# Optimization experiments

Measured on AMD Instinct MI355X. Metric: run time of the kernel, lower is better.

The kernel has to match this reference:

```python
import jax, jax.numpy as jnp
import numpy as np

GAMMA = 0.99
GAE_LAMBDA = 0.95
CLIP = 0.2
ENT_COEF = 0.01
VF_COEF = 0.5


def setup_inputs() -> dict:
    key = jax.random.key(0)
    ks = jax.random.split(key, 12)
    T, D, H, A = 65536, 512, 256, 16
    obs = jax.random.normal(ks[0], (T, D), dtype=jnp.float32)
    actions = jax.random.randint(ks[1], (T,), 0, A, dtype=jnp.int32)
    logprobs = jax.random.normal(ks[2], (T,), dtype=jnp.float32)
    rewards = jax.random.normal(ks[3], (T,), dtype=jnp.float32)
    terms = jax.random.uniform(ks[4], (T,), dtype=jnp.float32)
    values = jax.random.normal(ks[5], (T,), dtype=jnp.float32)
    # orthogonal-init-like scaling (std sqrt(2) for trunk, 0.01 actor, 1.0 critic)
    W1 = jax.random.normal(ks[6], (D, H), dtype=jnp.float32) * np.float32(np.sqrt(2.0 / D))
    b1 = jnp.zeros((H,), jnp.float32)
    W2 = jax.random.normal(ks[7], (H, H), dtype=jnp.float32) * np.float32(np.sqrt(2.0 / H))
    b2 = jnp.zeros((H,), jnp.float32)
    Wa = jax.random.normal(ks[8], (H, A), dtype=jnp.float32) * np.float32(0.01 / np.sqrt(H))
    ba = jnp.zeros((A,), jnp.float32)
    Wc = jax.random.normal(ks[9], (H, 1), dtype=jnp.float32) * np.float32(1.0 / np.sqrt(H))
    bc = jnp.zeros((1,), jnp.float32)
    return {"obs": obs, "actions": actions, "logprobs": logprobs, "rewards": rewards,
            "terms": terms, "values": values, "W1": W1, "b1": b1, "W2": W2, "b2": b2,
            "Wa": Wa, "ba": ba, "Wc": Wc, "bc": bc}


def reference(obs, actions, logprobs, rewards, terms, values,
              W1, b1, W2, b2, Wa, ba, Wc, bc):
    # ---- GAE (torch.no_grad in original -> stop_gradient) ----
    nonterm = 1.0 - terms                                   # [T]
    next_vals = jnp.concatenate([values[1:], jnp.zeros((1,), values.dtype)])
    delta = rewards + GAMMA * next_vals * nonterm - values  # [T]

    def step(carry, x):  # reverse recurrence a_t = d_t + g*l*nt_t * a_{t+1}
        d, nt = x
        g = d + GAMMA * GAE_LAMBDA * nt * carry
        return g, g

    _, adv = jax.lax.scan(step, jnp.float32(0.0), (delta, nonterm), reverse=True)
    adv = jax.lax.stop_gradient(adv)
    returns = adv + jax.lax.stop_gradient(values)
    vals_old = jax.lax.stop_gradient(values)

    # ---- actor-critic MLP (get_action_and_value) ----
    hidden = jnp.tanh(jnp.tanh(obs @ W1 + b1) @ W2 + b2)    # [T,256]
    logits = hidden @ Wa + ba                               # [T,A]
    logp = jax.nn.log_softmax(logits, axis=-1)
    newlp = jnp.take_along_axis(logp, actions[:, None].astype(jnp.int32), axis=1)[:, 0]
    entropy = -jnp.sum(jnp.exp(logp) * logp, axis=-1)       # [T]
    value = (hidden @ Wc + bc)[:, 0]                        # [T]

    # ---- clipped PPO losses (single full-batch minibatch) ----
    ratio = jnp.exp(newlp - logprobs)
    a = (adv - adv.mean()) / (adv.std() + 1e-8)
    pg_loss = jnp.maximum(-a * ratio, -a * jnp.clip(ratio, 1.0 - CLIP, 1.0 + CLIP)).mean()
    v_clipped = vals_old + jnp.clip(value - vals_old, -CLIP, CLIP)
    v_loss = 0.5 * jnp.maximum((value - returns) ** 2, (v_clipped - returns) ** 2).mean()
    loss = pg_loss - ENT_COEF * entropy.mean() + VF_COEF * v_loss
    return loss
```

## Files before the change

### kernel.cpp

```cpp
#include <hip/hip_runtime.h>


#define TT 65536

typedef float f32x4 __attribute__((ext_vector_type(4)));
typedef __bf16 bf16x8 __attribute__((ext_vector_type(8)));
typedef unsigned short u16x8 __attribute__((ext_vector_type(8)));

__device__ __forceinline__ unsigned short f2bf(float f) {
    unsigned int u = __float_as_uint(f);
    unsigned int r = (u + 0x7fffu + ((u >> 16) & 1u)) >> 16;
    return (unsigned short)r;
}

__device__ __forceinline__ float fast_tanh(float x) {
    float e = __expf(2.0f * x);
    return fmaf(-2.0f, __builtin_amdgcn_rcpf(e + 1.0f), 1.0f);
}

__device__ __forceinline__ void suffix_scan256(float* sC, float* sD, int i) {
    float c = sC[i], d = sD[i];
#pragma unroll
    for (int s = 1; s < 256; s <<= 1) {
        float c2 = 1.0f, d2 = 0.0f;
        if (i + s < 256) { c2 = sC[i + s]; d2 = sD[i + s]; }
        __syncthreads();
        d = d + c * d2;
        c = c * c2;
        sC[i] = c; sD[i] = d;
        __syncthreads();
    }
}

__device__ __forceinline__ void gae_cd(const float* rewards, const float* terms,
                                       const float* values, int t, float* c, float* d) {
    float nt = 1.0f - terms[t];
    float nv = (t + 1 < TT) ? values[t + 1] : 0.0f;
    *d = rewards[t] + 0.99f * nv * nt - values[t];
    *c = 0.99f * 0.95f * nt;
}

__global__ void k_prep_gae1(const float* __restrict__ W1, const float* __restrict__ W2,
                            const float* __restrict__ Wa, const float* __restrict__ Wc,
                            unsigned short* __restrict__ W1T, unsigned short* __restrict__ W2T,
                            unsigned short* __restrict__ WavT,
                            const float* __restrict__ rewards, const float* __restrict__ terms,
                            const float* __restrict__ values, float* __restrict__ aggC,
                            float* __restrict__ aggD) {
    if (blockIdx.x < 800) {
        int idx = blockIdx.x * 256 + threadIdx.x;
        if (idx < 131072) {
            int n = idx >> 9, k = idx & 511;
            W1T[idx] = f2bf(W1[k * 256 + n]);
        } else if (idx < 196608) {
            int i = idx - 131072;
            int n = i >> 8, k = i & 255;
            W2T[i] = f2bf(W2[k * 256 + n]);
        } else if (idx < 204800) {
            int i = idx - 196608;
            int r = i >> 8, k = i & 255;
            float v = (r < 16) ? Wa[k * 16 + r] : ((r == 16) ? Wc[k] : 0.0f);
            WavT[i] = f2bf(v);
        }
        return;
    }
    __shared__ float sC[256], sD[256];
    int i = threadIdx.x;
    int b = blockIdx.x - 800;
    int t = b * 256 + i;
    float c, d;
    gae_cd(rewards, terms, values, t, &c, &d);
    sC[i] = c; sD[i] = d;
    __syncthreads();
    suffix_scan256(sC, sD, i);
    if (i == 0) { aggC[b] = sC[0]; aggD[b] = sD[0]; }
}

__global__ void k_gae3(const float* __restrict__ rewards, const float* __restrict__ terms,
                       const float* __restrict__ values, const float* __restrict__ aggC,
                       const float* __restrict__ aggD, float* __restrict__ adv,
                       float* __restrict__ ret, float* __restrict__ sumP) {
    __shared__ float sC[256], sD[256];
    int i = threadIdx.x, b = blockIdx.x;
    sC[i] = aggC[i]; sD[i] = aggD[i];
    __syncthreads();
    suffix_scan256(sC, sD, i);
    float carry = (b < 255) ? sD[b + 1] : 0.0f;
    __syncthreads();

    int t = b * 256 + i;
    float c, d;
    gae_cd(rewards, terms, values, t, &c, &d);
    sC[i] = c; sD[i] = d;
    __syncthreads();
    suffix_scan256(sC, sD, i);
    float a = sD[i] + sC[i] * carry;
    adv[t] = a;
    ret[t] = a + values[t];
    __syncthreads();
    sC[i] = a; sD[i] = a * a;
    __syncthreads();
#pragma unroll
    for (int s = 128; s > 0; s >>= 1) {
        if (i < s) { sC[i] += sC[i + s]; sD[i] += sD[i + s]; }
        __syncthreads();
    }
    if (i == 0) { sumP[2 * b] = sC[0]; sumP[2 * b + 1] = sD[0]; }
}

__global__ __launch_bounds__(1024, 4) void k_mlp(
    const float* __restrict__ obs, const int* __restrict__ actions,
    const float* __restrict__ logprobs, const float* __restrict__ values,
    const float* __restrict__ b1, const float* __restrict__ b2,
    const float* __restrict__ ba, const float* __restrict__ bc,
    const unsigned short* __restrict__ W1T, const unsigned short* __restrict__ W2T,
    const unsigned short* __restrict__ WavT, const float* __restrict__ adv,
    const float* __restrict__ ret, const float* __restrict__ sumP,
    float* __restrict__ lossP) {
    __shared__ __align__(16) unsigned char SM[147456];
    unsigned short* smH = (unsigned short*)SM;
    unsigned short* smB2 = (unsigned short*)(SM + 131072);
    float* red = (float*)SM;

    const int tid = threadIdx.x;
    const int wid = tid >> 6;
    const int lane = tid & 63;
    const int cl = lane & 15;
    const int gg = lane >> 4;
    const int mw = wid >> 2;
    const int nw = wid & 3;
    const int bm0 = blockIdx.x * 256;

    const int srow = tid >> 2;
    const int sslot = tid & 3;
    const int sdst = srow * 32 + (((sslot ^ ((srow >> 1) & 3))) << 3);

    unsigned short* smB1b[2] = {(unsigned short*)SM, (unsigned short*)(SM + 16384)};
    unsigned short* smAb[2]  = {(unsigned short*)(SM + 32768), (unsigned short*)(SM + 49152)};

    const float* aSrc = obs + (size_t)(bm0 + srow) * 512 + sslot * 8;
    float4 ar0, ar1;
    u16x8 brf;
    ar0 = *(const float4*)(aSrc);
    ar1 = *(const float4*)(aSrc + 4);
    brf = *(const u16x8*)(W1T + srow * 512 + sslot * 8);

    float meanA, rstdA;
    {
        if (tid < 256) { red[tid] = sumP[2 * tid]; red[256 + tid] = sumP[2 * tid + 1]; }
        __syncthreads();
#pragma unroll
        for (int s = 128; s > 0; s >>= 1) {
            if (tid < s) { red[tid] += red[tid + s]; red[256 + tid] += red[256 + tid + s]; }
            __syncthreads();
        }
        meanA = red[0] * (1.0f / TT);
        float var = red[256] * (1.0f / TT) - meanA * meanA;
        rstdA = 1.0f / (sqrtf(fmaxf(var, 0.0f)) + 1e-8f);
        __syncthreads();
    }

    float b1v[4], b2v[4];
#pragma unroll
    for (int n = 0; n < 4; ++n) {
        int c = nw * 64 + n * 16 + cl;
        b1v[n] = b1[c];
        b2v[n] = b2[c];
    }
    const float bav = ba[cl];
    const float bc0 = bc[0];

    f32x4 acc[4][4];
#pragma unroll
    for (int m = 0; m < 4; ++m)
#pragma unroll
        for (int n = 0; n < 4; ++n) acc[m][n] = (f32x4){0.f, 0.f, 0.f, 0.f};

    auto cvtWriteA = [&](const float4& f0, const float4& f1, unsigned short* dst) {
        u16x8 cc;
        cc[0] = f2bf(f0.x); cc[1] = f2bf(f0.y); cc[2] = f2bf(f0.z); cc[3] = f2bf(f0.w);
        cc[4] = f2bf(f1.x); cc[5] = f2bf(f1.y); cc[6] = f2bf(f1.z); cc[7] = f2bf(f1.w);
        *(u16x8*)(dst + sdst) = cc;
    };

    cvtWriteA(ar0, ar1, smAb[0]);
    *(u16x8*)(smB1b[0] + sdst) = brf;
    __syncthreads();

    u16x8 b2rf;
#pragma unroll
    for (int t = 0; t < 16; ++t) {
        if (t < 15) {
            ar0 = *(const float4*)(aSrc + (t + 1) * 32);
            ar1 = *(const float4*)(aSrc + (t + 1) * 32 + 4);
            brf = *(const u16x8*)(W1T + srow * 512 + (t + 1) * 32 + sslot * 8);
        } else {
            b2rf = *(const u16x8*)(W2T + srow * 256 + sslot * 8);
        }
        bf16x8 av[4], bv[4];
#pragma unroll
        for (int m = 0; m < 4; ++m) {
            int ra = mw * 64 + m * 16 + cl;
            av[m] = *(const bf16x8*)&smAb[t & 1][ra * 32 + ((gg ^ ((ra >> 1) & 3)) << 3)];
        }
#pragma unroll
        for (int n = 0; n < 4; ++n) {
            int rb = nw * 64 + n * 16 + cl;
            bv[n] = *(const bf16x8*)&smB1b[t & 1][rb * 32 + ((gg ^ ((rb >> 1) & 3)) << 3)];
        }
#pragma unroll
        for (int m = 0; m < 4; ++m)
#pragma unroll
            for (int n = 0; n < 4; ++n)
                acc[m][n] = __builtin_amdgcn_mfma_f32_16x16x32_bf16(av[m], bv[n], acc[m][n], 0, 0, 0);
        if (t < 15) {
            cvtWriteA(ar0, ar1, smAb[(t + 1) & 1]);
            *(u16x8*)(smB1b[(t + 1) & 1] + sdst) = brf;
        }
        __syncthreads();
    }

#pragma unroll
    for (int m = 0; m < 4; ++m)
#pragma unroll
        for (int n = 0; n < 4; ++n)
#pragma unroll
            for (int j = 0; j < 4; ++j) {
                int r = mw * 64 + m * 16 + gg * 4 + j;
                int c = nw * 64 + n * 16 + cl;
                smH[r * 256 + (c ^ ((r & 7) << 3))] = f2bf(fast_tanh(acc[m][n][j] + b1v[n]));
                acc[m][n][j] = 0.0f;
            }
    *(u16x8*)(smB2 + sdst) = b2rf;
    __syncthreads();

    u16x8 wvrf;
#pragma unroll
    for (int t = 0; t < 8; ++t) {
        if (t < 7) b2rf = *(const u16x8*)(W2T + srow * 256 + (t + 1) * 32 + sslot * 8);
        else       wvrf = *(const u16x8*)(WavT + (tid >> 5) * 256 + (tid & 31) * 8);
        bf16x8 av[4], bv[4];
#pragma unroll
        for (int m = 0; m < 4; ++m) {
            int ra = mw * 64 + m * 16 + cl;
            av[m] = *(const bf16x8*)&smH[ra * 256 + ((t * 32 + gg * 8) ^ ((ra & 7) << 3))];
        }
#pragma unroll
        for (int n = 0; n < 4; ++n) {
            int rb = nw * 64 + n * 16 + cl;
            bv[n] = *(const bf16x8*)&smB2[rb * 32 + ((gg ^ ((rb >> 1) & 3)) << 3)];
        }
#pragma unroll
        for (int m = 0; m < 4; ++m)
#pragma unroll
            for (int n = 0; n < 4; ++n)
                acc[m][n] = __builtin_amdgcn_mfma_f32_16x16x32_bf16(av[m], bv[n], acc[m][n], 0, 0, 0);
        __syncthreads();
        if (t < 7) {
            *(u16x8*)(smB2 + sdst) = b2rf;
            __syncthreads();
        }
    }

#pragma unroll
    for (int m = 0; m < 4; ++m)
#pragma unroll
        for (int n = 0; n < 4; ++n)
#pragma unroll
            for (int j = 0; j < 4; ++j) {
                int r = mw * 64 + m * 16 + gg * 4 + j;
                int c = nw * 64 + n * 16 + cl;
                smH[r * 256 + (c ^ ((r & 7) << 3))] = f2bf(fast_tanh(acc[m][n][j] + b2v[n]));
            }
    {
        int wrow = tid >> 5, we = (tid & 31) * 8;
        *(u16x8*)(smB2 + wrow * 256 + (we ^ ((wrow & 7) << 3))) = wvrf;
    }
    __syncthreads();

    f32x4 acc_a = {0.f, 0.f, 0.f, 0.f}, acc_v = {0.f, 0.f, 0.f, 0.f};
#pragma unroll
    for (int kk = 0; kk < 8; ++kk) {
        int r = wid * 16 + cl;
        bf16x8 av = *(const bf16x8*)&smH[r * 256 + ((kk * 32 + gg * 8) ^ ((r & 7) << 3))];
        int ra2 = cl;
        bf16x8 bva = *(const bf16x8*)&smB2[ra2 * 256 + ((kk * 32 + gg * 8) ^ ((ra2 & 7) << 3))];
        int rv = 16 + cl;
        bf16x8 bvv = *(const bf16x8*)&smB2[rv * 256 + ((kk * 32 + gg * 8) ^ ((rv & 7) << 3))];
        acc_a = __builtin_amdgcn_mfma_f32_16x16x32_bf16(av, bva, acc_a, 0, 0, 0);
        acc_v = __builtin_amdgcn_mfma_f32_16x16x32_bf16(av, bvv, acc_v, 0, 0, 0);
    }

    float lsum = 0.0f;
    const int t0 = bm0 + wid * 16;
#pragma unroll
    for (int j = 0; j < 4; ++j) {
        int t = t0 + gg * 4 + j;
        float lg = acc_a[j] + bav;
        float mx = lg;
#pragma unroll
        for (int dd = 1; dd < 16; dd <<= 1) mx = fmaxf(mx, __shfl_xor(mx, dd));
        float ex = __expf(lg - mx);
        float se = ex;
#pragma unroll
        for (int dd = 1; dd < 16; dd <<= 1) se += __shfl_xor(se, dd);
        float ls = __logf(se);
        float lp = lg - mx - ls;
        float pl = __expf(lp) * lp;
        float ent = pl;
#pragma unroll
        for (int dd = 1; dd < 16; dd <<= 1) ent += __shfl_xor(ent, dd);
        ent = -ent;
        int act = actions[t];
        float newlp = __shfl(lp, (lane & 48) | act);
        float val = __shfl(acc_v[j], lane & 48) + bc0;

        float lpo = logprobs[t];
        float at = (adv[t] - meanA) * rstdA;
        float rt = ret[t];
        float vo = values[t];
        float ratio = __expf(newlp - lpo);
        float rcl = fminf(fmaxf(ratio, 0.8f), 1.2f);
        float pg = fmaxf(-at * ratio, -at * rcl);
        float vcl = vo + fminf(fmaxf(val - vo, -0.2f), 0.2f);
        float dv = val - rt, dvc = vcl - rt;
        float vl = fmaxf(dv * dv, dvc * dvc);
        if (cl == 0) lsum += pg - 0.01f * ent + 0.25f * vl;
    }
    lsum += __shfl_xor(lsum, 16);
    lsum += __shfl_xor(lsum, 32);
    __syncthreads();
    if (lane == 0) red[wid] = lsum;
    __syncthreads();
    if (tid == 0) {
        float s = 0.0f;
#pragma unroll
        for (int w = 0; w < 16; ++w) s += red[w];
        lossP[blockIdx.x] = s;
    }
}

__global__ void k_final(const float* __restrict__ lossP, float* __restrict__ out) {
    __shared__ float s[256];
    int i = threadIdx.x;
    s[i] = lossP[i];
    __syncthreads();
#pragma unroll
    for (int st = 128; st > 0; st >>= 1) {
        if (i < st) s[i] += s[i + st];
        __syncthreads();
    }
    if (i == 0) out[0] = s[0] * (1.0f / TT);
}

extern "C" void kernel_launch(void* const* d_in, const int* in_sizes, int n_in,
                              void* d_out, int out_size, void* d_ws, size_t ws_size,
                              hipStream_t stream) {
    const float* obs      = (const float*)d_in[0];
    const int*   actions  = (const int*)d_in[1];
    const float* logprobs = (const float*)d_in[2];
    const float* rewards  = (const float*)d_in[3];
    const float* terms    = (const float*)d_in[4];
    const float* values   = (const float*)d_in[5];
    const float* W1 = (const float*)d_in[6];
    const float* b1 = (const float*)d_in[7];
    const float* W2 = (const float*)d_in[8];
    const float* b2 = (const float*)d_in[9];
    const float* Wa = (const float*)d_in[10];
    const float* ba = (const float*)d_in[11];
    const float* Wc = (const float*)d_in[12];
    const float* bc = (const float*)d_in[13];

    char* ws = (char*)d_ws;
    unsigned short* W1T  = (unsigned short*)(ws + 0);
    unsigned short* W2T  = (unsigned short*)(ws + 262144);
    unsigned short* WavT = (unsigned short*)(ws + 393216);
    float* advp  = (float*)(ws + 409600);
    float* retp  = (float*)(ws + 671744);
    float* aggC  = (float*)(ws + 933888);
    float* aggD  = (float*)(ws + 934912);
    float* sumP  = (float*)(ws + 936960);
    float* lossP = (float*)(ws + 939072);

    k_prep_gae1<<<1056, 256, 0, stream>>>(W1, W2, Wa, Wc, W1T, W2T, WavT,
                                          rewards, terms, values, aggC, aggD);
    k_gae3<<<256, 256, 0, stream>>>(rewards, terms, values, aggC, aggD, advp, retp, sumP);
    k_mlp<<<256, 1024, 0, stream>>>(obs, actions, logprobs, values, b1, b2, ba, bc,
                                    W1T, W2T, WavT, advp, retp, sumP, lossP);
    k_final<<<1, 256, 0, stream>>>(lossP, (float*)d_out);
}
```

Measured before the change: 76.70 us.

## Halve MLP row tile and load GEMM operands directly from global memory

The MLP kernel now processes 128 rows per block instead of 256, launching 512 blocks so more CUs get work. The shared-memory staging of obs and weight tiles, with its double buffering and per-step barriers, is removed: each wave loads its A fragments from global memory, converts them to bf16 in registers, and reads W1T/W2T/WavT fragments straight from global or L2. Separate shared buffers hold the two hidden layers, and only 8 of 16 waves run the head stage. This trades shared-memory reuse and coalesced staging for fewer barriers and more parallelism, at the risk of redundant global and L2 traffic on weights and poorly coalesced obs reads.

```diff
diff --git a/kernel.cpp b/kernel.cpp
--- a/kernel.cpp
+++ b/kernel.cpp
@@ -117,10 +117,9 @@
     const unsigned short* __restrict__ WavT, const float* __restrict__ adv,
     const float* __restrict__ ret, const float* __restrict__ sumP,
     float* __restrict__ lossP) {
-    __shared__ __align__(16) unsigned char SM[147456];
-    unsigned short* smH = (unsigned short*)SM;
-    unsigned short* smB2 = (unsigned short*)(SM + 131072);
-    float* red = (float*)SM;
+    __shared__ __align__(16) unsigned short smH1[128 * 256];
+    __shared__ __align__(16) unsigned short smH2[128 * 256];
+    float* red = (float*)smH1;
 
     const int tid = threadIdx.x;
     const int wid = tid >> 6;
@@ -129,21 +128,7 @@
     const int gg = lane >> 4;
     const int mw = wid >> 2;
     const int nw = wid & 3;
-    const int bm0 = blockIdx.x * 256;
-
-    const int srow = tid >> 2;
-    const int sslot = tid & 3;
-    const int sdst = srow * 32 + (((sslot ^ ((srow >> 1) & 3))) << 3);
-
-    unsigned short* smB1b[2] = {(unsigned short*)SM, (unsigned short*)(SM + 16384)};
-    unsigned short* smAb[2]  = {(unsigned short*)(SM + 32768), (unsigned short*)(SM + 49152)};
-
-    const float* aSrc = obs + (size_t)(bm0 + srow) * 512 + sslot * 8;
-    float4 ar0, ar1;
-    u16x8 brf;
-    ar0 = *(const float4*)(aSrc);
-    ar1 = *(const float4*)(aSrc + 4);
-    brf = *(const u16x8*)(W1T + srow * 512 + sslot * 8);
+    const int bm0 = blockIdx.x * 128;
 
     float meanA, rstdA;
     {
@@ -170,172 +155,146 @@
     const float bav = ba[cl];
     const float bc0 = bc[0];
 
-    f32x4 acc[4][4];
-#pragma unroll
-    for (int m = 0; m < 4; ++m)
+    f32x4 acc[2][4];
+#pragma unroll
+    for (int m = 0; m < 2; ++m)
 #pragma unroll
         for (int n = 0; n < 4; ++n) acc[m][n] = (f32x4){0.f, 0.f, 0.f, 0.f};
 
-    auto cvtWriteA = [&](const float4& f0, const float4& f1, unsigned short* dst) {
-        u16x8 cc;
-        cc[0] = f2bf(f0.x); cc[1] = f2bf(f0.y); cc[2] = f2bf(f0.z); cc[3] = f2bf(f0.w);
-        cc[4] = f2bf(f1.x); cc[5] = f2bf(f1.y); cc[6] = f2bf(f1.z); cc[7] = f2bf(f1.w);
-        *(u16x8*)(dst + sdst) = cc;
-    };
-
-    cvtWriteA(ar0, ar1, smAb[0]);
-    *(u16x8*)(smB1b[0] + sdst) = brf;
-    __syncthreads();
-
-    u16x8 b2rf;
-#pragma unroll
-    for (int t = 0; t < 16; ++t) {
-        if (t < 15) {
-            ar0 = *(const float4*)(aSrc + (t + 1) * 32);
-            ar1 = *(const float4*)(aSrc + (t + 1) * 32 + 4);
-            brf = *(const u16x8*)(W1T + srow * 512 + (t + 1) * 32 + sslot * 8);
-        } else {
-            b2rf = *(const u16x8*)(W2T + srow * 256 + sslot * 8);
-        }
-        bf16x8 av[4], bv[4];
-#pragma unroll
-        for (int m = 0; m < 4; ++m) {
-            int ra = mw * 64 + m * 16 + cl;
-            av[m] = *(const bf16x8*)&smAb[t & 1][ra * 32 + ((gg ^ ((ra >> 1) & 3)) << 3)];
-        }
-#pragma unroll
-        for (int n = 0; n < 4; ++n) {
-            int rb = nw * 64 + n * 16 + cl;
-            bv[n] = *(const bf16x8*)&smB1b[t & 1][rb * 32 + ((gg ^ ((rb >> 1) & 3)) << 3)];
-        }
-#pragma unroll
-        for (int m = 0; m < 4; ++m)
+    {
+        const float* aBase = obs + (size_t)(bm0 + mw * 32 + cl) * 512 + gg * 8;
+        const unsigned short* bBase = W1T + (size_t)(nw * 64 + cl) * 512 + gg * 8;
+#pragma unroll
+        for (int kt = 0; kt < 16; ++kt) {
+            bf16x8 av[2], bv[4];
+#pragma unroll
+            for (int m = 0; m < 2; ++m) {
+                const float* p = aBase + m * 16 * 512 + kt * 32;
+                float4 f0 = *(const float4*)(p);
+                float4 f1 = *(const float4*)(p + 4);
+                u16x8 cc;
+                cc[0] = f2bf(f0.x); cc[1] = f2bf(f0.y); cc[2] = f2bf(f0.z); cc[3] = f2bf(f0.w);
+                cc[4] = f2bf(f1.x); cc[5] = f2bf(f1.y); cc[6] = f2bf(f1.z); cc[7] = f2bf(f1.w);
+                av[m] = *(bf16x8*)&cc;
+            }
 #pragma unroll
             for (int n = 0; n < 4; ++n)
-                acc[m][n] = __builtin_amdgcn_mfma_f32_16x16x32_bf16(av[m], bv[n], acc[m][n], 0, 0, 0);
-        if (t < 15) {
-            cvtWriteA(ar0, ar1, smAb[(t + 1) & 1]);
-            *(u16x8*)(smB1b[(t + 1) & 1] + sdst) = brf;
-        }
-        __syncthreads();
-    }
-
-#pragma unroll
-    for (int m = 0; m < 4; ++m)
+                bv[n] = *(const bf16x8*)(bBase + n * 16 * 512 + kt * 32);
+#pragma unroll
+            for (int m = 0; m < 2; ++m)
+#pragma unroll
+                for (int n = 0; n < 4; ++n)
+                    acc[m][n] = __builtin_amdgcn_mfma_f32_16x16x32_bf16(av[m], bv[n], acc[m][n], 0, 0, 0);
+        }
+    }
+
+#pragma unroll
+    for (int m = 0; m < 2; ++m)
 #pragma unroll
         for (int n = 0; n < 4; ++n)
 #pragma unroll
             for (int j = 0; j < 4; ++j) {
-                int r = mw * 64 + m * 16 + gg * 4 + j;
+                int r = mw * 32 + m * 16 + gg * 4 + j;
                 int c = nw * 64 + n * 16 + cl;
-                smH[r * 256 + (c ^ ((r & 7) << 3))] = f2bf(fast_tanh(acc[m][n][j] + b1v[n]));
+                smH1[r * 256 + (c ^ ((r & 7) << 3))] = f2bf(fast_tanh(acc[m][n][j] + b1v[n]));
                 acc[m][n][j] = 0.0f;
             }
-    *(u16x8*)(smB2 + sdst) = b2rf;
-    __syncthreads();
-
-    u16x8 wvrf;
-#pragma unroll
-    for (int t = 0; t < 8; ++t) {
-        if (t < 7) b2rf = *(const u16x8*)(W2T + srow * 256 + (t + 1) * 32 + sslot * 8);
-        else       wvrf = *(const u16x8*)(WavT + (tid >> 5) * 256 + (tid & 31) * 8);
-        bf16x8 av[4], bv[4];
-#pragma unroll
-        for (int m = 0; m < 4; ++m) {
-            int ra = mw * 64 + m * 16 + cl;
-            av[m] = *(const bf16x8*)&smH[ra * 256 + ((t * 32 + gg * 8) ^ ((ra & 7) << 3))];
-        }
-#pragma unroll
-        for (int n = 0; n < 4; ++n) {
-            int rb = nw * 64 + n * 16 + cl;
-            bv[n] = *(const bf16x8*)&smB2[rb * 32 + ((gg ^ ((rb >> 1) & 3)) << 3)];
-        }
-#pragma unroll
-        for (int m = 0; m < 4; ++m)
+    __syncthreads();
+
+    {
+        const unsigned short* bBase = W2T + (size_t)(nw * 64 + cl) * 256 + gg * 8;
+        const int ar0 = mw * 32 + cl;
+#pragma unroll
+        for (int kt = 0; kt < 8; ++kt) {
+            bf16x8 av[2], bv[4];
+#pragma unroll
+            for (int m = 0; m < 2; ++m) {
+                int r = ar0 + m * 16;
+                av[m] = *(const bf16x8*)&smH1[r * 256 + ((kt * 32 + gg * 8) ^ ((r & 7) << 3))];
+            }
 #pragma unroll
             for (int n = 0; n < 4; ++n)
-                acc[m][n] = __builtin_amdgcn_mfma_f32_16x16x32_bf16(av[m], bv[n], acc[m][n], 0, 0, 0);
-        __syncthreads();
-        if (t < 7) {
-            *(u16x8*)(smB2 + sdst) = b2rf;
-            __syncthreads();
-        }
-    }
-
-#pragma unroll
-    for (int m = 0; m < 4; ++m)
+                bv[n] = *(const bf16x8*)(bBase + n * 16 * 256 + kt * 32);
+#pragma unroll
+            for (int m = 0; m < 2; ++m)
+#pragma unroll
+                for (int n = 0; n < 4; ++n)
+                    acc[m][n] = __builtin_amdgcn_mfma_f32_16x16x32_bf16(av[m], bv[n], acc[m][n], 0, 0, 0);
+        }
+    }
+
+#pragma unroll
+    for (int m = 0; m < 2; ++m)
 #pragma unroll
         for (int n = 0; n < 4; ++n)
 #pragma unroll
             for (int j = 0; j < 4; ++j) {
-                int r = mw * 64 + m * 16 + gg * 4 + j;
+                int r = mw * 32 + m * 16 + gg * 4 + j;
                 int c = nw * 64 + n * 16 + cl;
-                smH[r * 256 + (c ^ ((r & 7) << 3))] = f2bf(fast_tanh(acc[m][n][j] + b2v[n]));
+                smH2[r * 256 + (c ^ ((r & 7) << 3))] = f2bf(fast_tanh(acc[m][n][j] + b2v[n]));
             }
-    {
-        int wrow = tid >> 5, we = (tid & 31) * 8;
-        *(u16x8*)(smB2 + wrow * 256 + (we ^ ((wrow & 7) << 3))) = wvrf;
-    }
-    __syncthreads();
-
-    f32x4 acc_a = {0.f, 0.f, 0.f, 0.f}, acc_v = {0.f, 0.f, 0.f, 0.f};
-#pragma unroll
-    for (int kk = 0; kk < 8; ++kk) {
-        int r = wid * 16 + cl;
-        bf16x8 av = *(const bf16x8*)&smH[r * 256 + ((kk * 32 + gg * 8) ^ ((r & 7) << 3))];
-        int ra2 = cl;
-        bf16x8 bva = *(const bf16x8*)&smB2[ra2 * 256 + ((kk * 32 + gg * 8) ^ ((ra2 & 7) << 3))];
-        int rv = 16 + cl;
-        bf16x8 bvv = *(const bf16x8*)&smB2[rv * 256 + ((kk * 32 + gg * 8) ^ ((rv & 7) << 3))];
-        acc_a = __builtin_amdgcn_mfma_f32_16x16x32_bf16(av, bva, acc_a, 0, 0, 0);
-        acc_v = __builtin_amdgcn_mfma_f32_16x16x32_bf16(av, bvv, acc_v, 0, 0, 0);
-    }
+    __syncthreads();
 
     float lsum = 0.0f;
-    const int t0 = bm0 + wid * 16;
-#pragma unroll
-    for (int j = 0; j < 4; ++j) {
-        int t = t0 + gg * 4 + j;
-        float lg = acc_a[j] + bav;
-        float mx = lg;
-#pragma unroll
-        for (int dd = 1; dd < 16; dd <<= 1) mx = fmaxf(mx, __shfl_xor(mx, dd));
-        float ex = __expf(lg - mx);
-        float se = ex;
-#pragma unroll
-        for (int dd = 1; dd < 16; dd <<= 1) se += __shfl_xor(se, dd);
-        float ls = __logf(se);
-        float lp = lg - mx - ls;
-        float pl = __expf(lp) * lp;
-        float ent = pl;
-#pragma unroll
-        for (int dd = 1; dd < 16; dd <<= 1) ent += __shfl_xor(ent, dd);
-        ent = -ent;
-        int act = actions[t];
-        float newlp = __shfl(lp, (lane & 48) | act);
-        float val = __shfl(acc_v[j], lane & 48) + bc0;
-
-        float lpo = logprobs[t];
-        float at = (adv[t] - meanA) * rstdA;
-        float rt = ret[t];
-        float vo = values[t];
-        float ratio = __expf(newlp - lpo);
-        float rcl = fminf(fmaxf(ratio, 0.8f), 1.2f);
-        float pg = fmaxf(-at * ratio, -at * rcl);
-        float vcl = vo + fminf(fmaxf(val - vo, -0.2f), 0.2f);
-        float dv = val - rt, dvc = vcl - rt;
-        float vl = fmaxf(dv * dv, dvc * dvc);
-        if (cl == 0) lsum += pg - 0.01f * ent + 0.25f * vl;
-    }
-    lsum += __shfl_xor(lsum, 16);
-    lsum += __shfl_xor(lsum, 32);
-    __syncthreads();
-    if (lane == 0) red[wid] = lsum;
+    if (wid < 8) {
+        f32x4 acc_a = {0.f, 0.f, 0.f, 0.f}, acc_v = {0.f, 0.f, 0.f, 0.f};
+        const unsigned short* baA = WavT + (size_t)cl * 256 + gg * 8;
+        const unsigned short* baV = WavT + (size_t)(16 + cl) * 256 + gg * 8;
+#pragma unroll
+        for (int kk = 0; kk < 8; ++kk) {
+            int r = wid * 16 + cl;
+            bf16x8 av = *(const bf16x8*)&smH2[r * 256 + ((kk * 32 + gg * 8) ^ ((r & 7) << 3))];
+            bf16x8 bva = *(const bf16x8*)(baA + kk * 32);
+            bf16x8 bvv = *(const bf16x8*)(baV + kk * 32);
+            acc_a = __builtin_amdgcn_mfma_f32_16x16x32_bf16(av, bva, acc_a, 0, 0, 0);
+            acc_v = __builtin_amdgcn_mfma_f32_16x16x32_bf16(av, bvv, acc_v, 0, 0, 0);
+        }
+
+        const int t0 = bm0 + wid * 16;
+#pragma unroll
+        for (int j = 0; j < 4; ++j) {
+            int t = t0 + gg * 4 + j;
+            float lg = acc_a[j] + bav;
+            float mx = lg;
+#pragma unroll
+            for (int dd = 1; dd < 16; dd <<= 1) mx = fmaxf(mx, __shfl_xor(mx, dd));
+            float ex = __expf(lg - mx);
+            float se = ex;
+#pragma unroll
+            for (int dd = 1; dd < 16; dd <<= 1) se += __shfl_xor(se, dd);
+            float ls = __logf(se);
+            float lp = lg - mx - ls;
+            float pl = __expf(lp) * lp;
+            float ent = pl;
+#pragma unroll
+            for (int dd = 1; dd < 16; dd <<= 1) ent += __shfl_xor(ent, dd);
+            ent = -ent;
+            int act = actions[t];
+            float newlp = __shfl(lp, (lane & 48) | act);
+            float val = __shfl(acc_v[j], lane & 48) + bc0;
+
+            float lpo = logprobs[t];
+            float at = (adv[t] - meanA) * rstdA;
+            float rt = ret[t];
+            float vo = values[t];
+            float ratio = __expf(newlp - lpo);
+            float rcl = fminf(fmaxf(ratio, 0.8f), 1.2f);
+            float pg = fmaxf(-at * ratio, -at * rcl);
+            float vcl = vo + fminf(fmaxf(val - vo, -0.2f), 0.2f);
+            float dv = val - rt, dvc = vcl - rt;
+            float vl = fmaxf(dv * dv, dvc * dvc);
+            if (cl == 0) lsum += pg - 0.01f * ent + 0.25f * vl;
+        }
+        lsum += __shfl_xor(lsum, 16);
+        lsum += __shfl_xor(lsum, 32);
+    }
+    __syncthreads();
+    if (wid < 8 && lane == 0) red[wid] = lsum;
     __syncthreads();
     if (tid == 0) {
         float s = 0.0f;
 #pragma unroll
-        for (int w = 0; w < 16; ++w) s += red[w];
+        for (int w = 0; w < 8; ++w) s += red[w];
         lossP[blockIdx.x] = s;
     }
 }
@@ -343,7 +302,7 @@
 __global__ void k_final(const float* __restrict__ lossP, float* __restrict__ out) {
     __shared__ float s[256];
     int i = threadIdx.x;
-    s[i] = lossP[i];
+    s[i] = lossP[i] + lossP[i + 256];
     __syncthreads();
 #pragma unroll
     for (int st = 128; st > 0; st >>= 1) {
@@ -385,7 +344,7 @@
     k_prep_gae1<<<1056, 256, 0, stream>>>(W1, W2, Wa, Wc, W1T, W2T, WavT,
                                           rewards, terms, values, aggC, aggD);
     k_gae3<<<256, 256, 0, stream>>>(rewards, terms, values, aggC, aggD, advp, retp, sumP);
-    k_mlp<<<256, 1024, 0, stream>>>(obs, actions, logprobs, values, b1, b2, ba, bc,
+    k_mlp<<<512, 1024, 0, stream>>>(obs, actions, logprobs, values, b1, b2, ba, bc,
                                     W1T, W2T, WavT, advp, retp, sumP, lossP);
     k_final<<<1, 256, 0, stream>>>(lossP, (float*)d_out);
 }
```

Result: slower. 176.4 us (+130.0%).
